# Kernel tuning notes

Hardware: AMD Instinct MI355X
Metric: run time of the kernel (lower is better)

The kernel has to match this reference:

```python
import jax, jax.numpy as jnp
import numpy as np
from jax import lax

NPOINTS = 1024   # centroids sampled by FPS
RADIUS = 0.2     # ball-query radius
K = 64           # max neighbors per centroid


def setup_inputs() -> dict:
    key = jax.random.key(0)
    ks = jax.random.split(key, 8)
    B, N, C = 8, 8192, 64
    pos = jax.random.uniform(ks[0], (B, N, 3), dtype=jnp.float32)
    feat = jax.random.normal(ks[1], (B, N, C), dtype=jnp.float32)
    w1 = jax.random.normal(ks[2], (C + 3, 64), dtype=jnp.float32) * 0.05
    b1 = jnp.zeros((64,), jnp.float32)
    w2 = jax.random.normal(ks[3], (64, 64), dtype=jnp.float32) * 0.05
    b2 = jnp.zeros((64,), jnp.float32)
    w3 = jax.random.normal(ks[4], (64, 128), dtype=jnp.float32) * 0.05
    b3 = jnp.zeros((128,), jnp.float32)
    return {"pos": pos, "feat": feat, "w1": w1, "b1": b1, "w2": w2, "b2": b2, "w3": w3, "b3": b3}


def fps(pos, npoints):
    """Iterative farthest point sampling; returns centroid indices [B, npoints]."""
    B, N, _ = pos.shape

    def step(carry, _):
        dist, far = carry
        centroid = jnp.take_along_axis(pos, far[:, None, None], axis=1)  # [B,1,3]
        d = jnp.sum((pos - centroid) ** 2, axis=-1)                       # [B,N]
        dist = jnp.minimum(dist, d)
        nxt = jnp.argmax(dist, axis=-1).astype(jnp.int32)
        return (dist, nxt), far

    init = (jnp.full((B, N), 1e10, jnp.float32), jnp.zeros((B,), jnp.int32))
    _, cent = lax.scan(step, init, None, length=npoints)  # [npoints, B]
    return cent.T  # [B, npoints]


def ball_group(pos, centroids, radius, k):
    """Radius ball query as in FixedRadiusNearNeighbors: mask->sort->clamp-to-first."""
    B, N, _ = pos.shape
    center = jnp.take_along_axis(pos, centroids[..., None], axis=1)  # [B,S,3]
    # squared distances [B,S,N] without materializing [B,S,N,3]
    sqr = (jnp.sum(center ** 2, -1)[:, :, None]
           + jnp.sum(pos ** 2, -1)[:, None, :]
           - 2.0 * jnp.einsum('bsd,bnd->bsn', center, pos))
    arang = jnp.arange(N, dtype=jnp.int32)[None, None, :]
    idx = jnp.where(sqr > radius ** 2, jnp.int32(N), arang)   # [B,S,N]
    idx = jnp.sort(idx, axis=-1)[:, :, :k]                     # [B,S,K]
    first = idx[:, :, :1]
    idx = jnp.where(idx == N, first, idx)
    return center, idx


def reference(pos, feat, w1, b1, w2, b2, w3, b3):
    B, N, C = feat.shape
    cent = fps(pos, NPOINTS)                                   # [B,S] int32
    center, gidx = ball_group(pos, cent, RADIUS, K)            # [B,S,3], [B,S,K]
    S = NPOINTS
    flat = gidx.reshape(B, S * K)
    gpos = jnp.take_along_axis(pos, flat[..., None], axis=1).reshape(B, S, K, 3)
    gfeat = jnp.take_along_axis(feat, flat[..., None], axis=1).reshape(B, S, K, C)
    # relative-position message concat grouped features (RelativePositionMessage)
    h = jnp.concatenate([gpos - center[:, :, None, :], gfeat], axis=-1)  # [B,S,K,C+3]
    h = jax.nn.relu(h @ w1 + b1)
    h = jax.nn.relu(h @ w2 + b2)
    h = jax.nn.relu(h @ w3 + b3)
    new_feat = jnp.max(h, axis=2)  # max-pool over neighbors -> [B,S,128]
    return center, new_feat
```

## Files before the change

kernel.cpp:

```cpp
#include <hip/hip_runtime.h>

#define NB 8
#define NN 8192
#define NC 64
#define NS 1024
#define KK 64

typedef unsigned long long u64;

template <int CTRL>
__device__ __forceinline__ u64 dpp_max_step(u64 k) {
  unsigned lo = (unsigned)k, hi = (unsigned)(k >> 32);
  unsigned plo = (unsigned)__builtin_amdgcn_update_dpp(0, (int)lo, CTRL, 0xF, 0xF, true);
  unsigned phi = (unsigned)__builtin_amdgcn_update_dpp(0, (int)hi, CTRL, 0xF, 0xF, true);
  u64 ok = ((u64)phi << 32) | plo;
  return ok > k ? ok : k;
}
#define DPP_XOR1 0xB1
#define DPP_XOR2 0x4E
#define DPP_HM   0x141
#define DPP_MIR  0x140

__device__ __forceinline__ u64 swz16_max(u64 k) {
  unsigned lo = (unsigned)k, hi = (unsigned)(k >> 32);
  unsigned plo = (unsigned)__builtin_amdgcn_ds_swizzle((int)lo, 0x401F);
  unsigned phi = (unsigned)__builtin_amdgcn_ds_swizzle((int)hi, 0x401F);
  u64 ok = ((u64)phi << 32) | plo;
  return ok > k ? ok : k;
}

__global__ __launch_bounds__(512) void fps_kernel(
    const float* __restrict__ pos, float* __restrict__ center_out)
{
#pragma clang fp contract(off)
  const int b = blockIdx.x;
  const int t = threadIdx.x;
  const int lane = t & 63;
  const int wid = t >> 6;
  const float* posb = pos + (size_t)b * (NN * 3);

  __shared__ u64 red[2][8];

  float px[16], py[16], pz[16], dist[16];
#pragma unroll
  for (int k = 0; k < 16; ++k) {
    int p = t + (k << 9);
    px[k] = posb[p * 3 + 0];
    py[k] = posb[p * 3 + 1];
    pz[k] = posb[p * 3 + 2];
    dist[k] = 1e10f;
  }
  float cx = posb[0], cy = posb[1], cz = posb[2];

  for (int it = 0; it < NS; ++it) {
    if (t == 0) {
      float* co = center_out + ((size_t)b * NS + it) * 3;
      co[0] = cx; co[1] = cy; co[2] = cz;
    }

    float bestv = -1.0f;
    int bestp = 0;
#pragma unroll
    for (int k = 0; k < 16; ++k) {
      float dx = px[k] - cx;
      float dy = py[k] - cy;
      float dz = pz[k] - cz;
      float d = ((dx * dx) + (dy * dy)) + (dz * dz);
      float nd = fminf(dist[k], d);
      dist[k] = nd;
      if (nd > bestv) { bestv = nd; bestp = t + (k << 9); }
    }

    u64 key = ((u64)__float_as_uint(bestv) << 32) | (unsigned)(8191 - bestp);
    key = dpp_max_step<DPP_XOR1>(key);
    key = dpp_max_step<DPP_XOR2>(key);
    key = dpp_max_step<DPP_HM>(key);
    key = dpp_max_step<DPP_MIR>(key);
    key = swz16_max(key);
    {
      u64 ok = __shfl_xor(key, 32);
      if (ok > key) key = ok;
    }
    if (lane == 0) red[it & 1][wid] = key;
    __syncthreads();

    u64 kw = red[it & 1][lane & 7];
    kw = dpp_max_step<DPP_XOR1>(kw);
    kw = dpp_max_step<DPP_XOR2>(kw);
    kw = dpp_max_step<DPP_HM>(kw);
    int win = 8191 - (int)(unsigned)kw;

    const float* wp = posb + (size_t)win * 3;
    cx = wp[0]; cy = wp[1]; cz = wp[2];
  }
}

__global__ __launch_bounds__(256) void ball_kernel(
    const float* __restrict__ pos, const float* __restrict__ center_out,
    int* __restrict__ gidx)
{
#pragma clang fp contract(off)
  const double R2D = 0.2 * 0.2;
  int sw = ((blockIdx.x & 7) << 8) | (blockIdx.x >> 3);
  int gw = (sw << 2) | ((int)threadIdx.x >> 6);
  int lane = threadIdx.x & 63;
  int b = gw >> 10;
  int s = gw & 1023;
  const float* posb = pos + (size_t)b * (NN * 3);
  const float* c = center_out + ((size_t)b * NS + s) * 3;
  double cx = (double)c[0], cy = (double)c[1], cz = (double)c[2];
  double cs = ((cx * cx) + (cy * cy)) + (cz * cz);
  int* out = gidx + ((size_t)b * NS + s) * KK;

  int count = 0;
  int first = -1;
  for (int base = 0; base < NN; base += 64) {
    if (count >= KK) break;
    int p = base + lane;
    double x = (double)posb[p * 3 + 0];
    double y = (double)posb[p * 3 + 1];
    double z = (double)posb[p * 3 + 2];
    double ps = ((x * x) + (y * y)) + (z * z);
    double dt = ((cx * x) + (cy * y)) + (cz * z);
    double sqr = (cs + ps) - (2.0 * dt);
    bool inr = !(sqr > R2D);
    u64 m = __ballot(inr);
    if (first < 0 && m) first = base + __builtin_ctzll(m);
    int pre = __popcll(m & ((1ull << lane) - 1ull));
    int slot = count + pre;
    if (inr && slot < KK) out[slot] = p;
    count += (int)__popcll(m);
  }
  if (count < KK) {
    for (int s2 = count + lane; s2 < KK; s2 += 64) out[s2] = first;
  }
}

__global__ __launch_bounds__(256) void mlp_kernel(
    const float* __restrict__ pos, const float* __restrict__ feat,
    const float* __restrict__ w1, const float* __restrict__ b1,
    const float* __restrict__ w2, const float* __restrict__ b2,
    const float* __restrict__ w3, const float* __restrict__ b3,
    const int* __restrict__ gidx, const float* __restrict__ center_out,
    float* __restrict__ out_feat)
{
  __shared__ float Xs[64][67];
  __shared__ float H1s[64][65];
  __shared__ float H2s[64][65];

  int bid = blockIdx.x;
  int bs = ((bid & 7) << 10) | (bid >> 3);
  int b = bs >> 10;
  int t = threadIdx.x;
  int p = t & 63;
  int q = __builtin_amdgcn_readfirstlane(t >> 6);

  int g = gidx[(size_t)bs * KK + p];
  const float* fp = feat + ((size_t)b * NN + g) * NC;
#pragma unroll
  for (int i = 0; i < 4; ++i) {
    float4 v = *(const float4*)(fp + q * 16 + i * 4);
    Xs[p][3 + q * 16 + i * 4 + 0] = v.x;
    Xs[p][3 + q * 16 + i * 4 + 1] = v.y;
    Xs[p][3 + q * 16 + i * 4 + 2] = v.z;
    Xs[p][3 + q * 16 + i * 4 + 3] = v.w;
  }
  if (q == 0) {
    const float* c = center_out + (size_t)bs * 3;
    const float* pp = pos + ((size_t)b * NN + g) * 3;
    Xs[p][0] = pp[0] - c[0];
    Xs[p][1] = pp[1] - c[1];
    Xs[p][2] = pp[2] - c[2];
  }
  __syncthreads();

  {
    int c0 = q * 16;
    float acc[16];
#pragma unroll
    for (int j = 0; j < 16; ++j) acc[j] = b1[c0 + j];
#pragma unroll 4
    for (int k = 0; k < 67; ++k) {
      float xv = Xs[p][k];
      const float4* wr = (const float4*)(w1 + (size_t)k * 64 + c0);
      float4 wa = wr[0], wb = wr[1], wc = wr[2], wd = wr[3];
      acc[0] = fmaf(xv, wa.x, acc[0]);   acc[1] = fmaf(xv, wa.y, acc[1]);
      acc[2] = fmaf(xv, wa.z, acc[2]);   acc[3] = fmaf(xv, wa.w, acc[3]);
      acc[4] = fmaf(xv, wb.x, acc[4]);   acc[5] = fmaf(xv, wb.y, acc[5]);
      acc[6] = fmaf(xv, wb.z, acc[6]);   acc[7] = fmaf(xv, wb.w, acc[7]);
      acc[8] = fmaf(xv, wc.x, acc[8]);   acc[9] = fmaf(xv, wc.y, acc[9]);
      acc[10] = fmaf(xv, wc.z, acc[10]); acc[11] = fmaf(xv, wc.w, acc[11]);
      acc[12] = fmaf(xv, wd.x, acc[12]); acc[13] = fmaf(xv, wd.y, acc[13]);
      acc[14] = fmaf(xv, wd.z, acc[14]); acc[15] = fmaf(xv, wd.w, acc[15]);
    }
#pragma unroll
    for (int j = 0; j < 16; ++j) H1s[p][c0 + j] = fmaxf(acc[j], 0.0f);
  }
  __syncthreads();

  {
    int c0 = q * 16;
    float acc[16];
#pragma unroll
    for (int j = 0; j < 16; ++j) acc[j] = b2[c0 + j];
#pragma unroll 4
    for (int k = 0; k < 64; ++k) {
      float xv = H1s[p][k];
      const float4* wr = (const float4*)(w2 + (size_t)k * 64 + c0);
      float4 wa = wr[0], wb = wr[1], wc = wr[2], wd = wr[3];
      acc[0] = fmaf(xv, wa.x, acc[0]);   acc[1] = fmaf(xv, wa.y, acc[1]);
      acc[2] = fmaf(xv, wa.z, acc[2]);   acc[3] = fmaf(xv, wa.w, acc[3]);
      acc[4] = fmaf(xv, wb.x, acc[4]);   acc[5] = fmaf(xv, wb.y, acc[5]);
      acc[6] = fmaf(xv, wb.z, acc[6]);   acc[7] = fmaf(xv, wb.w, acc[7]);
      acc[8] = fmaf(xv, wc.x, acc[8]);   acc[9] = fmaf(xv, wc.y, acc[9]);
      acc[10] = fmaf(xv, wc.z, acc[10]); acc[11] = fmaf(xv, wc.w, acc[11]);
      acc[12] = fmaf(xv, wd.x, acc[12]); acc[13] = fmaf(xv, wd.y, acc[13]);
      acc[14] = fmaf(xv, wd.z, acc[14]); acc[15] = fmaf(xv, wd.w, acc[15]);
    }
#pragma unroll
    for (int j = 0; j < 16; ++j) H2s[p][c0 + j] = fmaxf(acc[j], 0.0f);
  }
  __syncthreads();

  {
    int c1 = q * 32;
    float acc[32];
#pragma unroll
    for (int j = 0; j < 32; ++j) acc[j] = b3[c1 + j];
#pragma unroll 2
    for (int k = 0; k < 64; ++k) {
      float xv = H2s[p][k];
      const float4* wr = (const float4*)(w3 + (size_t)k * 128 + c1);
#pragma unroll
      for (int i = 0; i < 8; ++i) {
        float4 w = wr[i];
        acc[i * 4 + 0] = fmaf(xv, w.x, acc[i * 4 + 0]);
        acc[i * 4 + 1] = fmaf(xv, w.y, acc[i * 4 + 1]);
        acc[i * 4 + 2] = fmaf(xv, w.z, acc[i * 4 + 2]);
        acc[i * 4 + 3] = fmaf(xv, w.w, acc[i * 4 + 3]);
      }
    }
    float* o = out_feat + (size_t)bs * 128 + c1;
#pragma unroll
    for (int j = 0; j < 32; ++j) {
      float v = acc[j];
#pragma unroll
      for (int off = 32; off; off >>= 1) v = fmaxf(v, __shfl_xor(v, off));
      v = fmaxf(v, 0.0f);
      if (p == 0) o[j] = v;
    }
  }
}

extern "C" void kernel_launch(void* const* d_in, const int* in_sizes, int n_in,
                              void* d_out, int out_size, void* d_ws, size_t ws_size,
                              hipStream_t stream)
{
  (void)in_sizes; (void)n_in; (void)out_size; (void)ws_size;
  const float* pos = (const float*)d_in[0];
  const float* feat = (const float*)d_in[1];
  const float* w1 = (const float*)d_in[2];
  const float* b1 = (const float*)d_in[3];
  const float* w2 = (const float*)d_in[4];
  const float* b2 = (const float*)d_in[5];
  const float* w3 = (const float*)d_in[6];
  const float* b3 = (const float*)d_in[7];

  float* center_out = (float*)d_out;
  float* out_feat = (float*)d_out + (size_t)NB * NS * 3;
  int* gidx = (int*)d_ws;

  fps_kernel<<<NB, 512, 0, stream>>>(pos, center_out);
  ball_kernel<<<(NB * NS) / 4, 256, 0, stream>>>(pos, center_out, gidx);
  mlp_kernel<<<NB * NS, 256, 0, stream>>>(pos, feat, w1, b1, w2, b2, w3, b3,
                                          gidx, center_out, out_feat);
}
```

Baseline: 1.496 ms.

## Mirror FPS points in LDS, tree-reduce per-thread argmax, batch centroid writes

The FPS kernel now copies all point positions into shared memory as float4, so each iteration reads the winning centroid from LDS instead of global memory. Centroid coordinates are buffered in LDS and written out once after the loop rather than on every iteration. The per-thread argmax over 16 points is now a pairwise tree on packed 64-bit keys instead of a sequential compare chain, which shortens the dependency chain on the serial critical path. The change uses roughly 140KB of LDS per block, which limits occupancy to one block per CU; that is acceptable here since there are only 8 blocks.

```diff
diff --git a/kernel.cpp b/kernel.cpp
--- a/kernel.cpp
+++ b/kernel.cpp
@@ -39,49 +39,63 @@
   const int wid = t >> 6;
   const float* posb = pos + (size_t)b * (NN * 3);
 
+  __shared__ float pmir[NN * 4];
+  __shared__ float cent[NS * 3];
   __shared__ u64 red[2][8];
 
   float px[16], py[16], pz[16], dist[16];
 #pragma unroll
   for (int k = 0; k < 16; ++k) {
     int p = t + (k << 9);
-    px[k] = posb[p * 3 + 0];
-    py[k] = posb[p * 3 + 1];
-    pz[k] = posb[p * 3 + 2];
+    float x = posb[p * 3 + 0];
+    float y = posb[p * 3 + 1];
+    float z = posb[p * 3 + 2];
+    px[k] = x; py[k] = y; pz[k] = z;
     dist[k] = 1e10f;
+    *(float4*)&pmir[p * 4] = make_float4(x, y, z, 0.0f);
   }
   float cx = posb[0], cy = posb[1], cz = posb[2];
 
   for (int it = 0; it < NS; ++it) {
     if (t == 0) {
-      float* co = center_out + ((size_t)b * NS + it) * 3;
-      co[0] = cx; co[1] = cy; co[2] = cz;
-    }
-
-    float bestv = -1.0f;
-    int bestp = 0;
+      cent[it * 3 + 0] = cx; cent[it * 3 + 1] = cy; cent[it * 3 + 2] = cz;
+    }
+
+    float nd[16];
 #pragma unroll
     for (int k = 0; k < 16; ++k) {
       float dx = px[k] - cx;
       float dy = py[k] - cy;
       float dz = pz[k] - cz;
       float d = ((dx * dx) + (dy * dy)) + (dz * dz);
-      float nd = fminf(dist[k], d);
-      dist[k] = nd;
-      if (nd > bestv) { bestv = nd; bestp = t + (k << 9); }
-    }
-
-    u64 key = ((u64)__float_as_uint(bestv) << 32) | (unsigned)(8191 - bestp);
-    key = dpp_max_step<DPP_XOR1>(key);
-    key = dpp_max_step<DPP_XOR2>(key);
-    key = dpp_max_step<DPP_HM>(key);
-    key = dpp_max_step<DPP_MIR>(key);
-    key = swz16_max(key);
-    {
-      u64 ok = __shfl_xor(key, 32);
-      if (ok > key) key = ok;
-    }
-    if (lane == 0) red[it & 1][wid] = key;
+      float m = fminf(dist[k], d);
+      dist[k] = m;
+      nd[k] = m;
+    }
+
+    u64 key[16];
+#pragma unroll
+    for (int k = 0; k < 16; ++k) {
+      key[k] = ((u64)__float_as_uint(nd[k]) << 32)
+             | (unsigned)(8191 - (t + (k << 9)));
+    }
+#pragma unroll
+    for (int s = 8; s; s >>= 1) {
+#pragma unroll
+      for (int k = 0; k < 8; ++k) {
+        if (k < s) { if (key[k + s] > key[k]) key[k] = key[k + s]; }
+      }
+    }
+    u64 kk = key[0];
+
+    kk = dpp_max_step<DPP_XOR1>(kk);
+    kk = dpp_max_step<DPP_XOR2>(kk);
+    kk = dpp_max_step<DPP_HM>(kk);
+    kk = dpp_max_step<DPP_MIR>(kk);
+    kk = swz16_max(kk);
+    { u64 ok = __shfl_xor(kk, 32); if (ok > kk) kk = ok; }
+
+    if (lane == 0) red[it & 1][wid] = kk;
     __syncthreads();
 
     u64 kw = red[it & 1][lane & 7];
@@ -90,9 +104,13 @@
     kw = dpp_max_step<DPP_HM>(kw);
     int win = 8191 - (int)(unsigned)kw;
 
-    const float* wp = posb + (size_t)win * 3;
-    cx = wp[0]; cy = wp[1]; cz = wp[2];
-  }
+    float4 wp = *(const float4*)&pmir[win * 4];
+    cx = wp.x; cy = wp.y; cz = wp.z;
+  }
+
+  __syncthreads();
+  float* co = center_out + (size_t)b * NS * 3;
+  for (int i = t; i < NS * 3; i += 512) co[i] = cent[i];
 }
 
 __global__ __launch_bounds__(256) void ball_kernel(
```

Result: faster. 1.403 ms (-6.2%).
